# Performance work log

Hardware: AMD Instinct MI355X
Metric: run time of the kernel (lower is better)

The kernel has to match this reference:

```python
import jax, jax.numpy as jnp
import numpy as np

NUM_HEADS = 12
KEEP_RATE = 0.7


def setup_inputs() -> dict:
    key = jax.random.key(0)
    ks = jax.random.split(key, 5)
    B, N, C = 64, 197, 768
    x = jax.random.normal(ks[0], (B, N, C), dtype=jnp.float32)
    qkv_w = jax.random.normal(ks[1], (3 * C, C), dtype=jnp.float32) * (C ** -0.5)
    qkv_b = jax.random.normal(ks[2], (3 * C,), dtype=jnp.float32) * 0.02
    proj_w = jax.random.normal(ks[3], (C, C), dtype=jnp.float32) * (C ** -0.5)
    proj_b = jax.random.normal(ks[4], (C,), dtype=jnp.float32) * 0.02
    return {"x": x, "qkv_w": qkv_w, "qkv_b": qkv_b, "proj_w": proj_w, "proj_b": proj_b}


def reference(x, qkv_w, qkv_b, proj_w, proj_b):
    B, N, C = x.shape
    H = NUM_HEADS
    D = C // H
    scale = D ** -0.5
    # qkv projection: [B,N,3C] -> [3,B,H,N,D]
    qkv = (x @ qkv_w.T + qkv_b).reshape(B, N, 3, H, D).transpose(2, 0, 3, 1, 4)
    q, k, v = qkv[0], qkv[1], qkv[2]
    # full materialized attention (required for cls-row extraction)
    attn = jax.nn.softmax(jnp.einsum('bhqd,bhkd->bhqk', q, k) * scale, axis=-1)
    out = jnp.einsum('bhqk,bhkd->bqhd', attn, v).reshape(B, N, C)
    out = out @ proj_w.T + proj_b
    # EViT token pruning: cls-token attention over non-cls keys, head-averaged
    left_tokens = int(KEEP_RATE * (N - 1))  # 137
    cls_attn = attn[:, :, 0, 1:].mean(axis=1)  # [B, N-1]
    _, idx = jax.lax.top_k(cls_attn, left_tokens)  # sorted descending, like torch.topk
    index = jnp.broadcast_to(idx[:, :, None], (B, left_tokens, C))
    return (out, index, idx, cls_attn)
```

## Files before the change

kernel.cpp:

```cpp
#include <hip/hip_runtime.h>
#include <hip/hip_bf16.h>
#include <stdint.h>

constexpr int BATCH = 64;
constexpr int NTOK  = 197;
constexpr int CDIM  = 768;
constexpr int NH    = 12;
constexpr int HD    = 64;
constexpr int MROWS = BATCH * NTOK;
constexpr int MPAD  = 12800;
constexpr int NROWT = MPAD / 128;
constexpr int LEFT  = 137;
constexpr int KPAD  = 224;
constexpr int BH    = BATCH * NH;
constexpr int SPAD  = 208;

constexpr size_t OUT_OFF_OUT   = 0;
constexpr size_t OUT_OFF_INDEX = (size_t)BATCH * NTOK * CDIM;
constexpr size_t OUT_OFF_IDX   = OUT_OFF_INDEX + (size_t)BATCH * LEFT * CDIM;
constexpr size_t OUT_OFF_CLS   = OUT_OFF_IDX + (size_t)BATCH * LEFT;

constexpr size_t WS_CLSPH = 0;
constexpr size_t WS_CLSF  = WS_CLSPH + (size_t)BH * (NTOK - 1);
constexpr size_t WS_IDXI  = WS_CLSF  + (size_t)BATCH * (NTOK - 1);
constexpr size_t WS_Q0    = WS_IDXI  + (size_t)BATCH * LEFT;
constexpr size_t WS_XB    = WS_Q0  + (size_t)BATCH * CDIM;
constexpr size_t WS_WB    = WS_XB  + (size_t)MPAD * CDIM / 2;
constexpr size_t WS_PB    = WS_WB  + (size_t)3 * CDIM * CDIM / 2;
constexpr size_t WS_QB    = WS_PB  + (size_t)CDIM * CDIM / 2;
constexpr size_t WS_KB    = WS_QB  + (size_t)BH * NTOK * HD / 2;
constexpr size_t WS_VTB   = WS_KB  + (size_t)BH * NTOK * HD / 2;
constexpr size_t WS_AOB   = WS_VTB + (size_t)BH * HD * KPAD / 2;
constexpr size_t WS_U     = WS_AOB + (size_t)MPAD * CDIM / 2;
constexpr size_t WS_S     = WS_U   + (size_t)BH * CDIM;

typedef __attribute__((ext_vector_type(8))) short short8;
typedef __attribute__((ext_vector_type(4))) float floatx4;

__device__ __forceinline__ ushort f2bf(float x) {
    __hip_bfloat16 h = __float2bfloat16(x);
    return *(ushort*)&h;
}

__device__ __forceinline__ void load_lds16(const ushort* g, ushort* l) {
    __builtin_amdgcn_global_load_lds(
        (const __attribute__((address_space(1))) uint32_t*)(uintptr_t)g,
        (__attribute__((address_space(3))) uint32_t*)(uint32_t)(uintptr_t)l,
        16, 0, 0);
}

constexpr int X_N4  = MROWS * CDIM / 4;
constexpr int X_NP4 = MPAD * CDIM / 4;
constexpr int W_N4  = 3 * CDIM * CDIM / 4;
constexpr int P_N4  = CDIM * CDIM / 4;
constexpr int CAST_TOTAL = X_NP4 + W_N4 + P_N4;
constexpr int CASTB = CAST_TOTAL / 256;

__global__ __launch_bounds__(256) void prep_kernel(const float* __restrict__ x,
                                                   const float* __restrict__ qkv_w,
                                                   const float* __restrict__ proj_w,
                                                   const float* __restrict__ qkv_b,
                                                   ushort* __restrict__ xb,
                                                   ushort* __restrict__ wb,
                                                   ushort* __restrict__ pb,
                                                   float* __restrict__ U,
                                                   float* __restrict__ qbW) {
    const int bk = blockIdx.x;
    const int t  = threadIdx.x;

    if (bk < CASTB) {
        const int i = bk * 256 + t;
        const float* src; ushort* dst; int j, valid;
        if (i < X_NP4)             { src = x;      dst = xb; j = i;                valid = (j < X_N4); }
        else if (i < X_NP4 + W_N4) { src = qkv_w;  dst = wb; j = i - X_NP4;        valid = 1; }
        else                       { src = proj_w; dst = pb; j = i - X_NP4 - W_N4; valid = 1; }
        ushort4 h4 = make_ushort4(0, 0, 0, 0);
        if (valid) {
            float4 a = ((const float4*)src)[j];
            h4 = make_ushort4(f2bf(a.x), f2bf(a.y), f2bf(a.z), f2bf(a.w));
        }
        ((ushort4*)dst)[j] = h4;
        return;
    }

    const int bh = bk - CASTB;
    const int b  = bh / NH;
    const int h  = bh - b * NH;
    const int wv   = t >> 6;
    const int lane = t & 63;

    __shared__ float x0s[CDIM];
    __shared__ float q0s[HD];

    if (t < 192) ((float4*)x0s)[t] = ((const float4*)(x + (size_t)b * NTOK * CDIM))[t];
    __syncthreads();

    for (int i = 0; i < 16; ++i) {
        const int cl = wv * 16 + i;
        const int c  = h * HD + cl;
        const float* wr = qkv_w + (size_t)c * CDIM;
        float s = 0.f;
#pragma unroll
        for (int k = 0; k < 3; ++k) {
            float4 xv  = *(const float4*)(x0s + lane * 4 + k * 256);
            float4 wv4 = *(const float4*)(wr  + lane * 4 + k * 256);
            s += xv.x * wv4.x + xv.y * wv4.y + xv.z * wv4.z + xv.w * wv4.w;
        }
#pragma unroll
        for (int off = 32; off >= 1; off >>= 1) s += __shfl_xor(s, off);
        if (lane == 0) q0s[cl] = s + qkv_b[c];
    }
    __syncthreads();

    if (wv == 0) {
        float p = q0s[lane] * qkv_b[CDIM + h * HD + lane];
#pragma unroll
        for (int off = 32; off >= 1; off >>= 1) p += __shfl_xor(p, off);
        if (lane == 0) qbW[bh] = p;
    }

    const float* wk = qkv_w + (size_t)(CDIM + h * HD) * CDIM;
    float a0 = 0.f, a1 = 0.f, a2 = 0.f;
    for (int d = 0; d < HD; d++) {
        const float qd = q0s[d];
        const float* row = wk + (size_t)d * CDIM;
        a0 = fmaf(qd, row[t],       a0);
        a1 = fmaf(qd, row[t + 256], a1);
        a2 = fmaf(qd, row[t + 512], a2);
    }
    float* ub = U + (size_t)bh * CDIM;
    ub[t] = a0; ub[t + 256] = a1; ub[t + 512] = a2;
}

__global__ __launch_bounds__(512) void score_kernel(const float* __restrict__ x,
                                                    const float* __restrict__ U,
                                                    float* __restrict__ S) {
    const int b    = blockIdx.y;
    const int wv   = threadIdx.x >> 6;
    const int lane = threadIdx.x & 63;

    __shared__ float Us[NH][CDIM];
    for (int i = threadIdx.x; i < NH * (CDIM / 4); i += 512)
        ((float4*)Us)[i] = ((const float4*)(U + (size_t)b * NH * CDIM))[i];
    __syncthreads();

    const int j = blockIdx.x * 8 + wv;
    if (j >= NTOK) return;

    const float* xr = x + ((size_t)b * NTOK + j) * CDIM;
    float4 xv[3];
#pragma unroll
    for (int i = 0; i < 3; i++) xv[i] = *(const float4*)(xr + lane * 4 + i * 256);

    for (int h = 0; h < NH; h++) {
        const float* ur = Us[h];
        float s = 0.f;
#pragma unroll
        for (int i = 0; i < 3; i++) {
            float4 uv = *(const float4*)(ur + lane * 4 + i * 256);
            s += xv[i].x * uv.x + xv[i].y * uv.y + xv[i].z * uv.z + xv[i].w * uv.w;
        }
#pragma unroll
        for (int off = 32; off >= 1; off >>= 1) s += __shfl_xor(s, off);
        if (lane == 0) S[(size_t)(b * NH + h) * SPAD + j] = s;
    }
}

template <int MODE, int NCOLT>
__global__ __launch_bounds__(256, 4) void mfma_gemm128(
    const ushort* __restrict__ A, const ushort* __restrict__ W,
    const float* __restrict__ bias,
    float* __restrict__ O0f, ushort* __restrict__ O0q,
    ushort* __restrict__ O1k, ushort* __restrict__ O2vd,
    int Mvalid, int N) {
    constexpr int K   = CDIM;
    constexpr int BK  = 32;
    constexpr int NTK = K / BK;
    constexpr int nwg = NROWT * NCOLT;
    __shared__ ushort smem[16384];
    ushort* sA = smem;
    ushort* sB = smem + 8192;

    const int t    = threadIdx.x;
    const int lane = t & 63;
    const int w    = t >> 6;
    const int wm   = (w >> 1) * 64;
    const int wn   = (w & 1) * 64;
    const int fr   = lane & 15;
    const int fq   = lane >> 4;
    const int f3   = lane & 3;

    int row, col;
    {
        constexpr int q = nwg >> 3, r = nwg & 7;
        const int xcd = blockIdx.x & 7, lin = blockIdx.x >> 3;
        const int wg = (xcd < r ? xcd * (q + 1) : r * (q + 1) + (xcd - r) * q) + lin;
        row = wg / NCOLT; col = wg - row * NCOLT;
    }
    const int rowBase = row * 128;
    const int colBase = col * 128;

    auto stage = [&](const ushort* __restrict__ G, ushort* dst, int grow0, int kt) {
#pragma unroll
        for (int i = 0; i < 2; ++i) {
            const int l  = i * 256 + t;
            const int rl = l >> 2;
            const int sl = (l & 3) ^ (rl & 3);
            load_lds16(G + (size_t)(grow0 + rl) * K + kt * BK + sl * 8,
                       dst + l * 8);
        }
    };

    floatx4 acc[4][4];
#pragma unroll
    for (int i = 0; i < 4; ++i)
#pragma unroll
        for (int j = 0; j < 4; ++j)
#pragma unroll
            for (int r2 = 0; r2 < 4; ++r2) acc[i][j][r2] = 0.f;

    const int s0 = (fq ^ f3) * 8;

    stage(A, sA, rowBase, 0);
    stage(W, sB, colBase, 0);

    for (int kt = 0; kt < NTK; ++kt) {
        __syncthreads();
        const int cb = (kt & 1) << 12;
        if (kt + 1 < NTK) {
            stage(A, sA + (cb ^ 4096), rowBase, kt + 1);
            stage(W, sB + (cb ^ 4096), colBase, kt + 1);
        }

        const ushort* pa = sA + cb + (wm + fr) * BK;
        const ushort* pb = sB + cb + (wn + fr) * BK;
        short8 af[4], bf[4];
#pragma unroll
        for (int i = 0; i < 4; ++i) {
            af[i] = *(const short8*)(pa + i * 512 + s0);
            bf[i] = *(const short8*)(pb + i * 512 + s0);
        }
#pragma unroll
        for (int i = 0; i < 4; ++i)
#pragma unroll
            for (int j = 0; j < 4; ++j)
                acc[i][j] = __builtin_amdgcn_mfma_f32_16x16x32_bf16(
                    af[i], bf[j], acc[i][j], 0, 0, 0);
    }

    if (MODE == 0) {
#pragma unroll
        for (int j = 0; j < 4; ++j) {
            const int nn = colBase + wn + j * 16 + fr;
            const float bq = bias[nn];
#pragma unroll
            for (int i = 0; i < 4; ++i) {
                const int mb = rowBase + wm + i * 16 + fq * 4;
#pragma unroll
                for (int r2 = 0; r2 < 4; ++r2) {
                    const int mm = mb + r2;
                    if (mm < Mvalid) O0f[(size_t)mm * N + nn] = acc[i][j][r2] + bq;
                }
            }
        }
    } else {
        const int which = colBase / CDIM;
        const int nc0   = colBase - which * CDIM;
        const int hbase = nc0 >> 6;
        ushort (*T)[136] = (ushort (*)[136])smem;
        const int hpw = wm >> 6;
#pragma unroll
        for (int hp = 0; hp < 2; ++hp) {
            __syncthreads();
            if (hpw == hp) {
#pragma unroll
                for (int j = 0; j < 4; ++j) {
                    const int nl = wn + j * 16 + fr;
                    const float bq = bias[colBase + nl];
#pragma unroll
                    for (int i = 0; i < 4; ++i)
#pragma unroll
                        for (int r2 = 0; r2 < 4; ++r2)
                            T[i * 16 + fq * 4 + r2][nl] = f2bf(acc[i][j][r2] + bq);
                }
            }
            __syncthreads();
            const int rowH = rowBase + hp * 64;
            if (which < 2) {
                ushort* O = (which == 0) ? O0q : O1k;
#pragma unroll
                for (int it = 0; it < 4; ++it) {
                    const int run = it * 32 + (t >> 3);
                    const int lr  = run >> 1;
                    const int hh  = run & 1;
                    const int d0  = (t & 7) * 8;
                    const int mm  = rowH + lr;
                    if (mm < Mvalid) {
                        const int b   = mm / NTOK;
                        const int tok = mm - b * NTOK;
                        *(short8*)(O + (((size_t)(b * NH + hbase + hh) * NTOK + tok) * HD + d0)) =
                            *(const short8*)&T[lr][hh * 64 + d0];
                    }
                }
            } else {
#pragma unroll
                for (int it = 0; it < 4; ++it) {
                    const int lr = it * 16 + (t >> 4);
                    const int c8 = (t & 15) * 8;
                    const int mm = rowH + lr;
                    if (mm < Mvalid)
                        *(short8*)(O2vd + ((size_t)mm * CDIM + nc0 + c8)) =
                            *(const short8*)&T[lr][c8];
                }
            }
        }
    }
}

constexpr int FILLB    = 256;
constexpr int FILL_TOT = BATCH * LEFT * (CDIM / 4);

__global__ __launch_bounds__(256) void attn_mfma_kernel(const ushort* __restrict__ Qb,
                                                        const ushort* __restrict__ Kb,
                                                        const ushort* __restrict__ Vd,
                                                        ushort* __restrict__ AOb,
                                                        const int* __restrict__ idxI,
                                                        float* __restrict__ fillDst) {
    if (blockIdx.x >= BH) {
        const int fb = blockIdx.x - BH;
        for (int i = fb * 256 + (int)threadIdx.x; i < FILL_TOT; i += FILLB * 256) {
            const float v = (float)idxI[i / (CDIM / 4)];
            ((float4*)fillDst)[i] = make_float4(v, v, v, v);
        }
        return;
    }

    const int bh = blockIdx.x;
    const int b  = bh / NH;
    const int h  = bh - b * NH;
    const int t  = threadIdx.x;
    const int wv   = t >> 6;
    const int lane = t & 63;
    const int qc   = lane & 15;
    const int quad = lane >> 4;

    constexpr int VSTR = KPAD + 8;
    __shared__ ushort Vt[HD][VSTR];
    __shared__ ushort Pl[4][4][16][32];
    __shared__ float  alf[4][4][16], lf[4][4][16];

    {
        for (int idx = t; idx < NTOK * 8; idx += 256) {
            const int tok = idx >> 3;
            const int d0  = (idx & 7) * 8;
            const short8 v = *(const short8*)(
                Vd + ((size_t)(b * NTOK + tok)) * CDIM + h * HD + d0);
#pragma unroll
            for (int jj = 0; jj < 8; ++jj) Vt[d0 + jj][tok] = (ushort)v[jj];
        }
        for (int idx = t; idx < (KPAD - NTOK) * HD; idx += 256) {
            const int tok = NTOK + (idx >> 6);
            const int d   = idx & 63;
            Vt[d][tok] = 0;
        }
    }

    const ushort* Qh = Qb + (size_t)bh * NTOK * HD;
    const ushort* Kh = Kb + (size_t)bh * NTOK * HD;

    const int tile0 = (wv == 0) ? 0 : 4 + (wv - 1) * 3;
    const int ntv   = (wv == 0) ? 4 : 3;

    short8 qf[4][2];
#pragma unroll
    for (int ti = 0; ti < 4; ++ti) {
        if (ti < ntv) {
            const int qrow = min((tile0 + ti) * 16 + qc, NTOK - 1);
            qf[ti][0] = *(const short8*)(Qh + (size_t)qrow * HD + quad * 8);
            qf[ti][1] = *(const short8*)(Qh + (size_t)qrow * HD + 32 + quad * 8);
        }
    }

    floatx4 o[4][4];
#pragma unroll
    for (int ti = 0; ti < 4; ++ti)
#pragma unroll
        for (int s = 0; s < 4; ++s)
#pragma unroll
            for (int r = 0; r < 4; ++r) o[ti][s][r] = 0.f;
    float m[4], l[4];
#pragma unroll
    for (int ti = 0; ti < 4; ++ti) { m[ti] = -INFINITY; l[ti] = 0.f; }

    __syncthreads();

    for (int c0 = 0; c0 < NTOK; c0 += 32) {
        const int kr0 = min(c0 + qc, NTOK - 1);
        const int kr1 = min(c0 + 16 + qc, NTOK - 1);
        const short8 kf00 = *(const short8*)(Kh + (size_t)kr0 * HD + quad * 8);
        const short8 kf01 = *(const short8*)(Kh + (size_t)kr0 * HD + 32 + quad * 8);
        const short8 kf10 = *(const short8*)(Kh + (size_t)kr1 * HD + quad * 8);
        const short8 kf11 = *(const short8*)(Kh + (size_t)kr1 * HD + 32 + quad * 8);

#pragma unroll
        for (int ti = 0; ti < 4; ++ti) {
            if (ti >= ntv) continue;
            floatx4 s0 = {0.f, 0.f, 0.f, 0.f}, s1 = {0.f, 0.f, 0.f, 0.f};
            s0 = __builtin_amdgcn_mfma_f32_16x16x32_bf16(kf00, qf[ti][0], s0, 0, 0, 0);
            s0 = __builtin_amdgcn_mfma_f32_16x16x32_bf16(kf01, qf[ti][1], s0, 0, 0, 0);
            s1 = __builtin_amdgcn_mfma_f32_16x16x32_bf16(kf10, qf[ti][0], s1, 0, 0, 0);
            s1 = __builtin_amdgcn_mfma_f32_16x16x32_bf16(kf11, qf[ti][1], s1, 0, 0, 0);

            float sv[8];
            float mloc = -INFINITY;
#pragma unroll
            for (int r = 0; r < 4; ++r) {
                const int key0 = c0 + quad * 4 + r;
                const int key1 = key0 + 16;
                sv[r]     = (key0 < NTOK) ? s0[r] * 0.125f : -1e30f;
                sv[4 + r] = (key1 < NTOK) ? s1[r] * 0.125f : -1e30f;
                mloc = fmaxf(mloc, fmaxf(sv[r], sv[4 + r]));
            }
            mloc = fmaxf(mloc, __shfl_xor(mloc, 16));
            mloc = fmaxf(mloc, __shfl_xor(mloc, 32));
            const float mnew  = fmaxf(m[ti], mloc);
            const float alpha = __expf(m[ti] - mnew);
            float p[8], ps = 0.f;
#pragma unroll
            for (int i = 0; i < 8; ++i) { p[i] = __expf(sv[i] - mnew); ps += p[i]; }
            ps += __shfl_xor(ps, 16);
            ps += __shfl_xor(ps, 32);
            l[ti] = l[ti] * alpha + ps;
            m[ti] = mnew;

#pragma unroll
            for (int r = 0; r < 4; ++r) {
                Pl[wv][ti][qc][quad * 4 + r]      = f2bf(p[r]);
                Pl[wv][ti][qc][16 + quad * 4 + r] = f2bf(p[4 + r]);
            }
            if (quad == 0) alf[wv][ti][qc] = alpha;
        }
        __syncthreads();

        short8 pf[4];
#pragma unroll
        for (int ti = 0; ti < 4; ++ti) {
            if (ti >= ntv) continue;
            pf[ti] = *(const short8*)&Pl[wv][ti][qc][quad * 8];
            float ar[4];
#pragma unroll
            for (int r = 0; r < 4; ++r) ar[r] = alf[wv][ti][quad * 4 + r];
#pragma unroll
            for (int s = 0; s < 4; ++s)
#pragma unroll
                for (int r = 0; r < 4; ++r) o[ti][s][r] *= ar[r];
        }

#pragma unroll
        for (int s = 0; s < 4; ++s) {
            const short8 vf = *(const short8*)&Vt[s * 16 + qc][c0 + quad * 8];
#pragma unroll
            for (int ti = 0; ti < 4; ++ti)
                if (ti < ntv)
                    o[ti][s] = __builtin_amdgcn_mfma_f32_16x16x32_bf16(
                        pf[ti], vf, o[ti][s], 0, 0, 0);
        }
        __syncthreads();
    }

#pragma unroll
    for (int ti = 0; ti < 4; ++ti)
        if (ti < ntv && quad == 0) lf[wv][ti][qc] = l[ti];
    __syncthreads();

#pragma unroll
    for (int ti = 0; ti < 4; ++ti) {
        if (ti >= ntv) continue;
        const int qt = tile0 + ti;
#pragma unroll
        for (int r = 0; r < 4; ++r) {
            const int tok = qt * 16 + quad * 4 + r;
            if (tok >= NTOK) continue;
            const float inv = 1.f / lf[wv][ti][quad * 4 + r];
            ushort* dst = AOb + ((size_t)(b * NTOK + tok)) * CDIM + h * HD;
#pragma unroll
            for (int s = 0; s < 4; ++s) dst[s * 16 + qc] = f2bf(o[ti][s][r] * inv);
        }
    }
}

__global__ __launch_bounds__(256) void topk_fused_kernel(const float* __restrict__ S,
                                                         const float* __restrict__ qbW,
                                                         int* __restrict__ idxI,
                                                         float* __restrict__ idxOut,
                                                         float* __restrict__ outCls) {
    const int b    = blockIdx.x;
    const int t    = threadIdx.x;
    const int lane = t & 63;
    const int w    = t >> 6;

    __shared__ float qbv[NH];
    __shared__ float redm[4], reds[4];
    __shared__ float vsh[NTOK - 1];

    if (t < NH) qbv[t] = qbW[b * NH + t];
    __syncthreads();

    float macc = 0.f;
    for (int h = 0; h < NH; ++h) {
        const float qb = qbv[h];
        const float sv = (t < NTOK) ? (S[(size_t)(b * NH + h) * SPAD + t] + qb) * 0.125f
                                    : -INFINITY;
        float mloc = sv;
#pragma unroll
        for (int off = 32; off >= 1; off >>= 1) mloc = fmaxf(mloc, __shfl_xor(mloc, off));
        if (lane == 0) redm[w] = mloc;
        __syncthreads();
        const float mx = fmaxf(fmaxf(redm[0], redm[1]), fmaxf(redm[2], redm[3]));
        const float p = (t < NTOK) ? expf(sv - mx) : 0.f;
        float ls = p;
#pragma unroll
        for (int off = 32; off >= 1; off >>= 1) ls += __shfl_xor(ls, off);
        if (lane == 0) reds[w] = ls;
        __syncthreads();
        const float denom = (reds[0] + reds[1]) + (reds[2] + reds[3]);
        macc += p / denom;
        __syncthreads();
    }

    if (t >= 1 && t < NTOK) {
        const float val = macc * (1.f / 12.f);
        vsh[t - 1] = val;
        outCls[(size_t)b * (NTOK - 1) + (t - 1)] = val;
    }
    __syncthreads();

    if (t < NTOK - 1) {
        const float vi = vsh[t];
        int rank = 0;
        for (int j = 0; j < NTOK - 1; j++) {
            const float vj = vsh[j];
            rank += (vj > vi) || (vj == vi && j < t);
        }
        if (rank < LEFT) {
            idxI[b * LEFT + rank]   = t;
            idxOut[b * LEFT + rank] = (float)t;
        }
    }
}

extern "C" void kernel_launch(void* const* d_in, const int* in_sizes, int n_in,
                              void* d_out, int out_size, void* d_ws, size_t ws_size,
                              hipStream_t stream) {
    const float* x      = (const float*)d_in[0];
    const float* qkv_w  = (const float*)d_in[1];
    const float* qkv_b  = (const float*)d_in[2];
    const float* proj_w = (const float*)d_in[3];
    const float* proj_b = (const float*)d_in[4];
    float* out = (float*)d_out;

    float*  ws    = (float*)d_ws;
    int*    idxi  = (int*)(ws + WS_IDXI);
    float*  qbW   = ws + WS_Q0;
    ushort* xb    = (ushort*)(ws + WS_XB);
    ushort* wb    = (ushort*)(ws + WS_WB);
    ushort* pb    = (ushort*)(ws + WS_PB);
    ushort* qb    = (ushort*)(ws + WS_QB);
    ushort* kb    = (ushort*)(ws + WS_KB);
    ushort* vd    = (ushort*)(ws + WS_VTB);
    ushort* aob   = (ushort*)(ws + WS_AOB);
    float*  U     = ws + WS_U;
    float*  S     = ws + WS_S;

    prep_kernel<<<CASTB + BH, 256, 0, stream>>>(x, qkv_w, proj_w, qkv_b,
                                                xb, wb, pb, U, qbW);

    score_kernel<<<dim3((NTOK + 7) / 8, BATCH), 512, 0, stream>>>(x, U, S);

    topk_fused_kernel<<<BATCH, 256, 0, stream>>>(S, qbW, idxi,
                                                 out + OUT_OFF_IDX,
                                                 out + OUT_OFF_CLS);

    mfma_gemm128<1, 18><<<NROWT * 18, 256, 0, stream>>>(
        xb, wb, qkv_b, nullptr, qb, kb, vd, MROWS, 3 * CDIM);

    attn_mfma_kernel<<<BH + FILLB, 256, 0, stream>>>(qb, kb, vd, aob,
                                                     idxi, out + OUT_OFF_INDEX);

    mfma_gemm128<0, 6><<<NROWT * 6, 256, 0, stream>>>(
        aob, pb, proj_b, out + OUT_OFF_OUT, nullptr, nullptr, nullptr,
        MROWS, CDIM);
}
```

Baseline: 303.5 us.

## Fuse score and top-k kernels; stage proj GEMM output through LDS for vector stores

Merges the cls-score kernel and the softmax/top-k kernel into a single per-batch kernel that keeps the scores in shared memory, removing one launch and the global round trip of S. The tradeoff is that the score work now runs on only 64 blocks instead of 25x64, so it has less parallelism. Separately, the output-projection GEMM epilogue now stages fp32 results through LDS in two halves and writes coalesced float4 rows, replacing scattered scalar stores.

```diff
diff --git a/kernel.cpp b/kernel.cpp
--- a/kernel.cpp
+++ b/kernel.cpp
@@ -132,37 +132,87 @@
     ub[t] = a0; ub[t + 256] = a1; ub[t + 512] = a2;
 }
 
-__global__ __launch_bounds__(512) void score_kernel(const float* __restrict__ x,
-                                                    const float* __restrict__ U,
-                                                    float* __restrict__ S) {
-    const int b    = blockIdx.y;
-    const int wv   = threadIdx.x >> 6;
-    const int lane = threadIdx.x & 63;
+__global__ __launch_bounds__(512) void score_topk_kernel(const float* __restrict__ x,
+                                                         const float* __restrict__ U,
+                                                         const float* __restrict__ qbW,
+                                                         int* __restrict__ idxI,
+                                                         float* __restrict__ idxOut,
+                                                         float* __restrict__ outCls) {
+    const int b    = blockIdx.x;
+    const int t    = threadIdx.x;
+    const int wv   = t >> 6;
+    const int lane = t & 63;
 
     __shared__ float Us[NH][CDIM];
-    for (int i = threadIdx.x; i < NH * (CDIM / 4); i += 512)
+    __shared__ float Ssh[NH][200];
+    __shared__ float qbv[NH];
+    __shared__ float redm[4], reds[4];
+    __shared__ float vsh[NTOK - 1];
+
+    for (int i = t; i < NH * (CDIM / 4); i += 512)
         ((float4*)Us)[i] = ((const float4*)(U + (size_t)b * NH * CDIM))[i];
-    __syncthreads();
-
-    const int j = blockIdx.x * 8 + wv;
-    if (j >= NTOK) return;
-
-    const float* xr = x + ((size_t)b * NTOK + j) * CDIM;
-    float4 xv[3];
-#pragma unroll
-    for (int i = 0; i < 3; i++) xv[i] = *(const float4*)(xr + lane * 4 + i * 256);
-
-    for (int h = 0; h < NH; h++) {
-        const float* ur = Us[h];
-        float s = 0.f;
-#pragma unroll
-        for (int i = 0; i < 3; i++) {
-            float4 uv = *(const float4*)(ur + lane * 4 + i * 256);
-            s += xv[i].x * uv.x + xv[i].y * uv.y + xv[i].z * uv.z + xv[i].w * uv.w;
-        }
-#pragma unroll
-        for (int off = 32; off >= 1; off >>= 1) s += __shfl_xor(s, off);
-        if (lane == 0) S[(size_t)(b * NH + h) * SPAD + j] = s;
+    if (t < NH) qbv[t] = qbW[b * NH + t];
+    __syncthreads();
+
+    for (int j = wv; j < NTOK; j += 8) {
+        const float* xr = x + ((size_t)b * NTOK + j) * CDIM;
+        float4 xv[3];
+#pragma unroll
+        for (int i = 0; i < 3; i++) xv[i] = *(const float4*)(xr + lane * 4 + i * 256);
+        for (int h = 0; h < NH; h++) {
+            const float* ur = Us[h];
+            float s = 0.f;
+#pragma unroll
+            for (int i = 0; i < 3; i++) {
+                float4 uv = *(const float4*)(ur + lane * 4 + i * 256);
+                s += xv[i].x * uv.x + xv[i].y * uv.y + xv[i].z * uv.z + xv[i].w * uv.w;
+            }
+#pragma unroll
+            for (int off = 32; off >= 1; off >>= 1) s += __shfl_xor(s, off);
+            if (lane == 0) Ssh[h][j] = s;
+        }
+    }
+    __syncthreads();
+
+    float macc = 0.f;
+    for (int h = 0; h < NH; ++h) {
+        const float qb = qbv[h];
+        const float sv = (t < NTOK) ? (Ssh[h][t] + qb) * 0.125f : -INFINITY;
+        float mloc = sv;
+#pragma unroll
+        for (int off = 32; off >= 1; off >>= 1) mloc = fmaxf(mloc, __shfl_xor(mloc, off));
+        if (lane == 0 && wv < 4) redm[wv] = mloc;
+        __syncthreads();
+        const float mx = fmaxf(fmaxf(redm[0], redm[1]), fmaxf(redm[2], redm[3]));
+        const float p = (t < NTOK) ? expf(sv - mx) : 0.f;
+        float ls = p;
+#pragma unroll
+        for (int off = 32; off >= 1; off >>= 1) ls += __shfl_xor(ls, off);
+        if (lane == 0 && wv < 4) reds[wv] = ls;
+        __syncthreads();
+        const float denom = (reds[0] + reds[1]) + (reds[2] + reds[3]);
+        macc += p / denom;
+        __syncthreads();
+    }
+
+    if (t >= 1 && t < NTOK) {
+        const float val = macc * (1.f / 12.f);
+        vsh[t - 1] = val;
+        outCls[(size_t)b * (NTOK - 1) + (t - 1)] = val;
+    }
+    __syncthreads();
+
+    if (t < NTOK - 1) {
+        const float vi = vsh[t];
+        int rank = 0;
+        for (int j = 0; j < NTOK - 1; j++) {
+            const float vj = vsh[j];
+            rank += (vj > vi) || (vj == vi && j < t);
+        }
+        if (rank < LEFT) {
+            idxI[b * LEFT + rank]   = t;
+            idxOut[b * LEFT + rank] = (float)t;
+        }
     }
 }
 
@@ -248,19 +298,34 @@
                     af[i], bf[j], acc[i][j], 0, 0, 0);
     }
 
+    const int hpw = wm >> 6;
     if (MODE == 0) {
-#pragma unroll
-        for (int j = 0; j < 4; ++j) {
-            const int nn = colBase + wn + j * 16 + fr;
-            const float bq = bias[nn];
-#pragma unroll
-            for (int i = 0; i < 4; ++i) {
-                const int mb = rowBase + wm + i * 16 + fq * 4;
-#pragma unroll
-                for (int r2 = 0; r2 < 4; ++r2) {
-                    const int mm = mb + r2;
-                    if (mm < Mvalid) O0f[(size_t)mm * N + nn] = acc[i][j][r2] + bq;
+        float (*Tf)[128] = (float (*)[128])smem;
+#pragma unroll
+        for (int hp = 0; hp < 2; ++hp) {
+            __syncthreads();
+            if (hpw == hp) {
+#pragma unroll
+                for (int j = 0; j < 4; ++j) {
+                    const int nl = wn + j * 16 + fr;
+                    const float bq = bias[colBase + nl];
+#pragma unroll
+                    for (int i = 0; i < 4; ++i)
+#pragma unroll
+                        for (int r2 = 0; r2 < 4; ++r2)
+                            Tf[i * 16 + fq * 4 + r2][nl] = acc[i][j][r2] + bq;
                 }
+            }
+            __syncthreads();
+            const int rowH = rowBase + hp * 64;
+#pragma unroll
+            for (int it = 0; it < 8; ++it) {
+                const int lr = it * 8 + (t >> 5);
+                const int c4 = (t & 31) * 4;
+                const int mm = rowH + lr;
+                if (mm < Mvalid)
+                    *(float4*)(O0f + (size_t)mm * N + colBase + c4) =
+                        *(const float4*)&Tf[lr][c4];
             }
         }
     } else {
@@ -268,7 +333,6 @@
         const int nc0   = colBase - which * CDIM;
         const int hbase = nc0 >> 6;
         ushort (*T)[136] = (ushort (*)[136])smem;
-        const int hpw = wm >> 6;
 #pragma unroll
         for (int hp = 0; hp < 2; ++hp) {
             __syncthreads();
@@ -489,66 +553,6 @@
     }
 }
 
-__global__ __launch_bounds__(256) void topk_fused_kernel(const float* __restrict__ S,
-                                                         const float* __restrict__ qbW,
-                                                         int* __restrict__ idxI,
-                                                         float* __restrict__ idxOut,
-                                                         float* __restrict__ outCls) {
-    const int b    = blockIdx.x;
-    const int t    = threadIdx.x;
-    const int lane = t & 63;
-    const int w    = t >> 6;
-
-    __shared__ float qbv[NH];
-    __shared__ float redm[4], reds[4];
-    __shared__ float vsh[NTOK - 1];
-
-    if (t < NH) qbv[t] = qbW[b * NH + t];
-    __syncthreads();
-
-    float macc = 0.f;
-    for (int h = 0; h < NH; ++h) {
-        const float qb = qbv[h];
-        const float sv = (t < NTOK) ? (S[(size_t)(b * NH + h) * SPAD + t] + qb) * 0.125f
-                                    : -INFINITY;
-        float mloc = sv;
-#pragma unroll
-        for (int off = 32; off >= 1; off >>= 1) mloc = fmaxf(mloc, __shfl_xor(mloc, off));
-        if (lane == 0) redm[w] = mloc;
-        __syncthreads();
-        const float mx = fmaxf(fmaxf(redm[0], redm[1]), fmaxf(redm[2], redm[3]));
-        const float p = (t < NTOK) ? expf(sv - mx) : 0.f;
-        float ls = p;
-#pragma unroll
-        for (int off = 32; off >= 1; off >>= 1) ls += __shfl_xor(ls, off);
-        if (lane == 0) reds[w] = ls;
-        __syncthreads();
-        const float denom = (reds[0] + reds[1]) + (reds[2] + reds[3]);
-        macc += p / denom;
-        __syncthreads();
-    }
-
-    if (t >= 1 && t < NTOK) {
-        const float val = macc * (1.f / 12.f);
-        vsh[t - 1] = val;
-        outCls[(size_t)b * (NTOK - 1) + (t - 1)] = val;
-    }
-    __syncthreads();
-
-    if (t < NTOK - 1) {
-        const float vi = vsh[t];
-        int rank = 0;
-        for (int j = 0; j < NTOK - 1; j++) {
-            const float vj = vsh[j];
-            rank += (vj > vi) || (vj == vi && j < t);
-        }
-        if (rank < LEFT) {
-            idxI[b * LEFT + rank]   = t;
-            idxOut[b * LEFT + rank] = (float)t;
-        }
-    }
-}
-
 extern "C" void kernel_launch(void* const* d_in, const int* in_sizes, int n_in,
                               void* d_out, int out_size, void* d_ws, size_t ws_size,
                               hipStream_t stream) {
@@ -570,14 +574,11 @@
     ushort* vd    = (ushort*)(ws + WS_VTB);
     ushort* aob   = (ushort*)(ws + WS_AOB);
     float*  U     = ws + WS_U;
-    float*  S     = ws + WS_S;
 
     prep_kernel<<<CASTB + BH, 256, 0, stream>>>(x, qkv_w, proj_w, qkv_b,
                                                 xb, wb, pb, U, qbW);
 
-    score_kernel<<<dim3((NTOK + 7) / 8, BATCH), 512, 0, stream>>>(x, U, S);
-
-    topk_fused_kernel<<<BATCH, 256, 0, stream>>>(S, qbW, idxi,
+    score_topk_kernel<<<BATCH, 512, 0, stream>>>(x, U, qbW, idxi,
                                                  out + OUT_OFF_IDX,
                                                  out + OUT_OFF_CLS);
 
```

Result: slower. 358.4 us (+18.1%).
